# Optimization experiments

Measured on AMD Instinct MI355X. Metric: run time of the kernel, lower is better.

Reference implementation:

```python
import jax, jax.numpy as jnp
import numpy as np

B, T = 2048, 512
IN, H1, H2, D1 = 1, 128, 64, 25


def _lstm_layer(x, w_ih, w_hh, b_ih, b_hh):
    """PyTorch-style LSTM layer. x: [B,T,in], returns hidden seq [B,T,H].
    Gate order (PyTorch): i, f, g, o."""
    Bb = x.shape[0]
    H = w_hh.shape[1]
    # Precompute input projections for all timesteps: [B,T,4H]
    x_proj = jnp.einsum('bti,gi->btg', x, w_ih) + b_ih + b_hh

    def step(carry, xt):
        h, c = carry  # [B,H] each
        gates = xt + h @ w_hh.T  # [B,4H]
        i, f, g, o = jnp.split(gates, 4, axis=-1)
        i = jax.nn.sigmoid(i)
        f = jax.nn.sigmoid(f)
        g = jnp.tanh(g)
        o = jax.nn.sigmoid(o)
        c = f * c + i * g
        h = o * jnp.tanh(c)
        return (h, c), h

    h0 = jnp.zeros((Bb, H), x.dtype)
    c0 = jnp.zeros((Bb, H), x.dtype)
    (_, _), hs = jax.lax.scan(step, (h0, c0), jnp.swapaxes(x_proj, 0, 1))
    return jnp.swapaxes(hs, 0, 1)  # [B,T,H]


def setup_inputs() -> dict:
    key = jax.random.key(0)
    ks = jax.random.split(key, 13)
    s1 = 1.0 / np.sqrt(H1)
    s2 = 1.0 / np.sqrt(H2)
    sd1 = 1.0 / np.sqrt(H2)
    sd2 = 1.0 / np.sqrt(D1)
    u = lambda k, shape, s: jax.random.uniform(k, shape, jnp.float32, -s, s)
    return {
        'x': jax.random.normal(ks[0], (B, T, IN), jnp.float32),
        'w_ih1': u(ks[1], (4 * H1, IN), s1),
        'w_hh1': u(ks[2], (4 * H1, H1), s1),
        'b_ih1': u(ks[3], (4 * H1,), s1),
        'b_hh1': u(ks[4], (4 * H1,), s1),
        'w_ih2': u(ks[5], (4 * H2, H1), s2),
        'w_hh2': u(ks[6], (4 * H2, H2), s2),
        'b_ih2': u(ks[7], (4 * H2,), s2),
        'b_hh2': u(ks[8], (4 * H2,), s2),
        'w_d1': u(ks[9], (D1, H2), sd1),
        'b_d1': u(ks[10], (D1,), sd1),
        'w_d2': u(ks[11], (1, D1), sd2),
        'b_d2': u(ks[12], (1,), sd2),
    }


def reference(x, w_ih1, w_hh1, b_ih1, b_hh1, w_ih2, w_hh2, b_ih2, b_hh2,
              w_d1, b_d1, w_d2, b_d2):
    out = _lstm_layer(x, w_ih1, w_hh1, b_ih1, b_hh1)   # [B,T,128]
    out = _lstm_layer(out, w_ih2, w_hh2, b_ih2, b_hh2)  # [B,T,64]
    last = out[:, -1, :]                                 # [B,64]
    h = last @ w_d1.T + b_d1                             # [B,25]
    y = h @ w_d2.T + b_d2                                # [B,1]
    return y
```

## Files before the change

### kernel.cpp

```cpp
#include <hip/hip_runtime.h>

#define TS 512
#define LOG2E 1.4426950408889634f

typedef _Float16 f16x8 __attribute__((ext_vector_type(8)));
typedef float f32x4 __attribute__((ext_vector_type(4)));

#define MFMA16(a, b, c) __builtin_amdgcn_mfma_f32_16x16x32_f16((a), (b), (c), 0, 0, 0)

__global__ __launch_bounds__(512) void prep(
    const float* __restrict__ w_hh1, const float* __restrict__ w_ih2,
    const float* __restrict__ w_hh2, _Float16* __restrict__ wsh)
{
  int idx = blockIdx.x * 512 + threadIdx.x;
  if (idx >= 114688) return;
  int slot = idx >> 3, j = idx & 7;
  float v;
  if (slot < 8192) {
    int l = slot & 63, fi = slot >> 6;
    int w = fi >> 5, f = fi & 31, tau = f >> 2, kt = f & 3;
    int n = (tau >> 1) * 128 + w * 32 + (tau & 1) * 16 + (l & 15);
    int k = kt * 32 + (l >> 4) * 8 + j;
    v = w_hh1[n * 128 + k];
  } else {
    int s2 = slot - 8192;
    int l = s2 & 63, fi = s2 >> 6;
    int w2 = fi / 24, f = fi % 24, g = f / 6, kt = f % 6;
    int n = g * 64 + w2 * 16 + (l & 15);
    int k = kt * 32 + (l >> 4) * 8 + j;
    v = (k < 128) ? w_ih2[n * 128 + k] : w_hh2[n * 64 + (k - 128)];
  }
  wsh[idx] = (_Float16)(v * LOG2E);
}

__device__ __forceinline__ float rcpf_(float x) { return __builtin_amdgcn_rcpf(x); }
__device__ __forceinline__ float sig_s(float s)  { return rcpf_(1.0f + exp2f(-s)); }
__device__ __forceinline__ float tanh_s(float s) { return 1.0f - 2.0f * rcpf_(exp2f(s + s) + 1.0f); }
__device__ __forceinline__ float tanh_c(float c) { return 1.0f - 2.0f * rcpf_(exp2f(c * (2.0f * LOG2E)) + 1.0f); }


#define L1_BODY(I, PI, PIM)                                                    \
  {                                                                            \
    f16x8 a0 = *(const f16x8*)((PIM) + lofs);                                  \
    f16x8 a1 = *(const f16x8*)((PIM) + lofs + 1024);                           \
    f16x8 a2 = *(const f16x8*)((PIM) + lofs + 2048);                           \
    f16x8 a3 = *(const f16x8*)((PIM) + lofs + 3072);                           \
    f32x4 acc[8];                                                              \
    _Pragma("unroll") for (int tau = 0; tau < 8; ++tau) {                      \
      acc[tau] = (f32x4){biv[tau], biv[tau], biv[tau], biv[tau]};              \
      acc[tau] = MFMA16(a0, BF[tau * 4 + 0], acc[tau]);                        \
      acc[tau] = MFMA16(a1, BF[tau * 4 + 1], acc[tau]);                        \
      acc[tau] = MFMA16(a2, BF[tau * 4 + 2], acc[tau]);                        \
      acc[tau] = MFMA16(a3, BF[tau * 4 + 3], acc[tau]);                        \
    }                                                                          \
    const float xv0 = x_lds[(rb + 0) * 516 + (I)];                             \
    const float xv1 = x_lds[(rb + 1) * 516 + (I)];                             \
    _Pragma("unroll") for (int c = 0; c < 2; ++c) {                            \
      _Pragma("unroll") for (int rr = 0; rr < 2; ++rr) {                       \
        const float xv = rr ? xv1 : xv0;                                       \
        float sv[4];                                                           \
        _Pragma("unroll") for (int g = 0; g < 4; ++g) {                        \
          const int tau = g * 2 + c;                                           \
          const float oth = __shfl_xor(acc[tau][2 + rr], 32, 64);              \
          const float mine = acc[tau][rr];                                     \
          sv[g] = fmaf(xv, wxv[tau], up ? oth : mine);                         \
        }                                                                      \
        const float ii = sig_s(sv[0]), ff = sig_s(sv[1]);                      \
        const float gv = tanh_s(sv[2]), oo = sig_s(sv[3]);                     \
        const int ci = c * 2 + rr;                                             \
        cst[ci] = fmaf(ff, cst[ci], ii * gv);                                  \
        const float hv = oo * tanh_c(cst[ci]);                                 \
        *(_Float16*)((PI) + ha[ci]) = (_Float16)hv;                            \
      }                                                                        \
    }                                                                          \
  }

#define L2_BODY(PI, PIM, WRLDS, WRF)                                           \
  {                                                                            \
    f16x8 e0 = *(const f16x8*)((PIM) + lofs);                                  \
    f16x8 e1 = *(const f16x8*)((PIM) + lofs + 1024);                           \
    f16x8 e2 = *(const f16x8*)((PIM) + lofs + 2048);                           \
    f16x8 e3 = *(const f16x8*)((PIM) + lofs + 3072);                           \
    f16x8 e4 = *(const f16x8*)((PI) + lofs + 4096);                            \
    f16x8 e5 = *(const f16x8*)((PI) + lofs + 5120);                            \
    f32x4 acc[4];                                                              \
    _Pragma("unroll") for (int g = 0; g < 4; ++g) {                            \
      acc[g] = (f32x4){biv[g], biv[g], biv[g], biv[g]};                        \
      acc[g] = MFMA16(e0, BF[g * 6 + 0], acc[g]);                              \
      acc[g] = MFMA16(e1, BF[g * 6 + 1], acc[g]);                              \
      acc[g] = MFMA16(e2, BF[g * 6 + 2], acc[g]);                              \
      acc[g] = MFMA16(e3, BF[g * 6 + 3], acc[g]);                              \
      acc[g] = MFMA16(e4, BF[g * 6 + 4], acc[g]);                              \
      acc[g] = MFMA16(e5, BF[g * 6 + 5], acc[g]);                              \
    }                                                                          \
    _Pragma("unroll") for (int rr = 0; rr < 2; ++rr) {                         \
      float sv[4];                                                             \
      _Pragma("unroll") for (int g = 0; g < 4; ++g) {                          \
        const float oth = __shfl_xor(acc[g][2 + rr], 32, 64);                  \
        const float mine = acc[g][rr];                                         \
        sv[g] = up ? oth : mine;                                               \
      }                                                                        \
      const float ii = sig_s(sv[0]), ff = sig_s(sv[1]);                        \
      const float gv = tanh_s(sv[2]), oo = sig_s(sv[3]);                       \
      cst[rr] = fmaf(ff, cst[rr], ii * gv);                                    \
      const float hv = oo * tanh_c(cst[rr]);                                   \
      if (WRLDS) *(_Float16*)((PIM) + ha[rr]) = (_Float16)hv;                  \
      if (WRF) h2f[rb + rr][w2 * 16 + col] = hv;                               \
    }                                                                          \
  }

__global__ __launch_bounds__(512, 2) void lstm_mfma(
    const float* __restrict__ x,
    const float* __restrict__ w_ih1,
    const float* __restrict__ b_ih1, const float* __restrict__ b_hh1,
    const float* __restrict__ b_ih2, const float* __restrict__ b_hh2,
    const float* __restrict__ w_d1, const float* __restrict__ b_d1,
    const float* __restrict__ w_d2, const float* __restrict__ b_d2,
    const _Float16* __restrict__ wsh,
    float* __restrict__ out)
{
  __shared__ __align__(16) _Float16 HC[2 * 3072];
  __shared__ __align__(16) float x_lds[8 * 516];
  __shared__ float h2f[8][65];
  __shared__ float dh[200];

  const int tid = threadIdx.x;
  const int w   = tid >> 6;
  const int l   = tid & 63;
  const int col = l & 15;
  const int qh  = (l >> 4) & 1;
  const int up  = l >> 5;
  const int rb  = 4 * qh + 2 * up;
  const int wg  = w >> 2;
  const int w2  = w & 3;
  const int r0  = blockIdx.x * 8;
  const int lofs = l * 16;

  f16x8 BF[32];
  float biv[8], wxv[8];
  int ha[4];

  if (wg == 0) {
    #pragma unroll
    for (int f = 0; f < 32; ++f)
      BF[f] = *(const f16x8*)(wsh + ((w * 32 + f) * 64 + l) * 8);
    #pragma unroll
    for (int tau = 0; tau < 8; ++tau) {
      int u = (tau >> 1) * 128 + w * 32 + (tau & 1) * 16 + col;
      biv[tau] = (b_ih1[u] + b_hh1[u]) * LOG2E;
      wxv[tau] = w_ih1[u] * LOG2E;
    }
    #pragma unroll
    for (int c = 0; c < 2; ++c)
      #pragma unroll
      for (int rr = 0; rr < 2; ++rr) {
        int u = w * 32 + c * 16 + col;
        int r = rb + rr;
        ha[c * 2 + rr] = (u >> 5) * 1024 + (r + ((u >> 3) & 3) * 16) * 16 + (u & 7) * 2;
      }
  } else {
    #pragma unroll
    for (int f = 0; f < 24; ++f)
      BF[f] = *(const f16x8*)(wsh + 65536 + ((w2 * 24 + f) * 64 + l) * 8);
    #pragma unroll
    for (int g = 0; g < 4; ++g) {
      int u = g * 64 + w2 * 16 + col;
      biv[g] = (b_ih2[u] + b_hh2[u]) * LOG2E;
    }
    #pragma unroll
    for (int rr = 0; rr < 2; ++rr) {
      int u2 = w2 * 16 + col;
      int r = rb + rr;
      ha[rr] = (4 + (u2 >> 5)) * 1024 + (r + ((u2 >> 3) & 3) * 16) * 16 + (u2 & 7) * 2;
    }
  }

  {
    int r = tid >> 6, cc = (tid & 63) * 8;
    const float4* src = (const float4*)(x + (r0 + r) * 512 + cc);
    float4 v0 = src[0], v1 = src[1];
    *(float4*)(x_lds + r * 516 + cc)     = v0;
    *(float4*)(x_lds + r * 516 + cc + 4) = v1;
  }
  for (int i2 = tid; i2 < 3072; i2 += 512) ((unsigned*)HC)[i2] = 0u;

  float cst[4] = {0.f, 0.f, 0.f, 0.f};
  char* const hcb = (char*)HC;
  __syncthreads();

  #pragma unroll 1
  for (int i = 0; i < TS; i += 2) {
    if (wg == 0)      { L1_BODY(i, hcb, hcb + 6144) }
    else if (i > 0)   { L2_BODY(hcb, hcb + 6144, 1, 0) }
    __syncthreads();
    if (wg == 0)      { L1_BODY(i + 1, hcb + 6144, hcb) }
    else              { L2_BODY(hcb + 6144, hcb, 1, 0) }
    __syncthreads();
  }
  if (wg == 1)        { L2_BODY(hcb, hcb + 6144, 0, 1) }
  __syncthreads();

  if (tid < 200) {
    int r = tid / 25, d = tid - r * 25;
    float acc = b_d1[d];
    #pragma unroll
    for (int uu = 0; uu < 64; ++uu) acc = fmaf(h2f[r][uu], w_d1[d * 64 + uu], acc);
    dh[tid] = acc;
  }
  __syncthreads();
  if (tid < 8) {
    float y = b_d2[0];
    #pragma unroll
    for (int d = 0; d < 25; ++d) y = fmaf(dh[tid * 25 + d], w_d2[d], y);
    out[r0 + tid] = y;
  }
}

extern "C" void kernel_launch(void* const* d_in, const int* in_sizes, int n_in,
                              void* d_out, int out_size, void* d_ws, size_t ws_size,
                              hipStream_t stream) {
  (void)in_sizes; (void)n_in; (void)out_size; (void)ws_size;
  const float* x     = (const float*)d_in[0];
  const float* w_ih1 = (const float*)d_in[1];
  const float* w_hh1 = (const float*)d_in[2];
  const float* b_ih1 = (const float*)d_in[3];
  const float* b_hh1 = (const float*)d_in[4];
  const float* w_ih2 = (const float*)d_in[5];
  const float* w_hh2 = (const float*)d_in[6];
  const float* b_ih2 = (const float*)d_in[7];
  const float* b_hh2 = (const float*)d_in[8];
  const float* w_d1  = (const float*)d_in[9];
  const float* b_d1  = (const float*)d_in[10];
  const float* w_d2  = (const float*)d_in[11];
  const float* b_d2  = (const float*)d_in[12];
  _Float16* wsh = (_Float16*)d_ws;
  float* outp = (float*)d_out;

  prep<<<224, 512, 0, stream>>>(w_hh1, w_ih2, w_hh2, wsh);
  lstm_mfma<<<256, 512, 0, stream>>>(x, w_ih1, b_ih1, b_hh1, b_ih2, b_hh2,
                                     w_d1, b_d1, w_d2, b_d2, wsh, outp);
}
```

Before: 564.4 us.

## Split layer-1 across 8 waves and fold input projection and bias into MFMA

Layer 1 now runs on 8 waves instead of 4, each owning 16 hidden units, so blocks grow to 768 threads with 3 blocks per CU targeted. The scalar x*w_ih + bias term is folded into one extra MFMA by packing (1, x) as fp16 in LDS, with a prepped weight fragment holding bias and w_ih. This halves per-wave register and serial work on the layer-1 critical path and removes per-step FMA work. The cost is bias and x now rounded to fp16, more waves contending per barrier, and higher register pressure limits at 768 threads.

```diff
diff --git a/kernel.cpp b/kernel.cpp
--- a/kernel.cpp
+++ b/kernel.cpp
@@ -5,27 +5,34 @@
 
 typedef _Float16 f16x8 __attribute__((ext_vector_type(8)));
 typedef float f32x4 __attribute__((ext_vector_type(4)));
+typedef unsigned int u32;
 
 #define MFMA16(a, b, c) __builtin_amdgcn_mfma_f32_16x16x32_f16((a), (b), (c), 0, 0, 0)
 
 __global__ __launch_bounds__(512) void prep(
-    const float* __restrict__ w_hh1, const float* __restrict__ w_ih2,
-    const float* __restrict__ w_hh2, _Float16* __restrict__ wsh)
+    const float* __restrict__ w_hh1, const float* __restrict__ w_ih1,
+    const float* __restrict__ b_ih1, const float* __restrict__ b_hh1,
+    const float* __restrict__ w_ih2, const float* __restrict__ w_hh2,
+    _Float16* __restrict__ wsh)
 {
   int idx = blockIdx.x * 512 + threadIdx.x;
-  if (idx >= 114688) return;
-  int slot = idx >> 3, j = idx & 7;
+  int l = (idx >> 3) & 63, j = idx & 7;
   float v;
-  if (slot < 8192) {
-    int l = slot & 63, fi = slot >> 6;
-    int w = fi >> 5, f = fi & 31, tau = f >> 2, kt = f & 3;
-    int n = (tau >> 1) * 128 + w * 32 + (tau & 1) * 16 + (l & 15);
+  if (idx < 65536) {
+    int f = idx >> 9;
+    int wi = f >> 4, g = (f >> 2) & 3, kt = f & 3;
+    int n = g * 128 + wi * 16 + (l & 15);
     int k = kt * 32 + (l >> 4) * 8 + j;
     v = w_hh1[n * 128 + k];
+  } else if (idx < 81920) {
+    int f = (idx - 65536) >> 9;
+    int wi = f >> 2, g = f & 3;
+    int n = g * 128 + wi * 16 + (l & 15);
+    int s = (l >> 4) * 8 + j;
+    v = (s == 0) ? (b_ih1[n] + b_hh1[n]) : ((s == 1) ? w_ih1[n] : 0.0f);
   } else {
-    int s2 = slot - 8192;
-    int l = s2 & 63, fi = s2 >> 6;
-    int w2 = fi / 24, f = fi % 24, g = f / 6, kt = f % 6;
+    int f = (idx - 81920) >> 9;
+    int w2 = f / 24, rem = f % 24, g = rem / 6, kt = rem % 6;
     int n = g * 64 + w2 * 16 + (l & 15);
     int k = kt * 32 + (l >> 4) * 8 + j;
     v = (k < 128) ? w_ih2[n * 128 + k] : w_hh2[n * 64 + (k - 128)];
@@ -41,78 +48,66 @@
 
 #define L1_BODY(I, PI, PIM)                                                    \
   {                                                                            \
-    f16x8 a0 = *(const f16x8*)((PIM) + lofs);                                  \
-    f16x8 a1 = *(const f16x8*)((PIM) + lofs + 1024);                           \
-    f16x8 a2 = *(const f16x8*)((PIM) + lofs + 2048);                           \
-    f16x8 a3 = *(const f16x8*)((PIM) + lofs + 3072);                           \
-    f32x4 acc[8];                                                              \
-    _Pragma("unroll") for (int tau = 0; tau < 8; ++tau) {                      \
-      acc[tau] = (f32x4){biv[tau], biv[tau], biv[tau], biv[tau]};              \
-      acc[tau] = MFMA16(a0, BF[tau * 4 + 0], acc[tau]);                        \
-      acc[tau] = MFMA16(a1, BF[tau * 4 + 1], acc[tau]);                        \
-      acc[tau] = MFMA16(a2, BF[tau * 4 + 2], acc[tau]);                        \
-      acc[tau] = MFMA16(a3, BF[tau * 4 + 3], acc[tau]);                        \
-    }                                                                          \
-    const float xv0 = x_lds[(rb + 0) * 516 + (I)];                             \
-    const float xv1 = x_lds[(rb + 1) * 516 + (I)];                             \
-    _Pragma("unroll") for (int c = 0; c < 2; ++c) {                            \
-      _Pragma("unroll") for (int rr = 0; rr < 2; ++rr) {                       \
-        const float xv = rr ? xv1 : xv0;                                       \
-        float sv[4];                                                           \
-        _Pragma("unroll") for (int g = 0; g < 4; ++g) {                        \
-          const int tau = g * 2 + c;                                           \
-          const float oth = __shfl_xor(acc[tau][2 + rr], 32, 64);              \
-          const float mine = acc[tau][rr];                                     \
-          sv[g] = fmaf(xv, wxv[tau], up ? oth : mine);                         \
-        }                                                                      \
-        const float ii = sig_s(sv[0]), ff = sig_s(sv[1]);                      \
-        const float gv = tanh_s(sv[2]), oo = sig_s(sv[3]);                     \
-        const int ci = c * 2 + rr;                                             \
-        cst[ci] = fmaf(ff, cst[ci], ii * gv);                                  \
-        const float hv = oo * tanh_c(cst[ci]);                                 \
-        *(_Float16*)((PI) + ha[ci]) = (_Float16)hv;                            \
-      }                                                                        \
-    }                                                                          \
-  }
-
-#define L2_BODY(PI, PIM, WRLDS, WRF)                                           \
-  {                                                                            \
-    f16x8 e0 = *(const f16x8*)((PIM) + lofs);                                  \
-    f16x8 e1 = *(const f16x8*)((PIM) + lofs + 1024);                           \
-    f16x8 e2 = *(const f16x8*)((PIM) + lofs + 2048);                           \
-    f16x8 e3 = *(const f16x8*)((PIM) + lofs + 3072);                           \
-    f16x8 e4 = *(const f16x8*)((PI) + lofs + 4096);                            \
-    f16x8 e5 = *(const f16x8*)((PI) + lofs + 5120);                            \
+    union { u32 uu[4]; f16x8 vv; } a6u;                                        \
+    a6u.uu[0] = xpk[xrow + (I)];                                               \
+    a6u.uu[1] = 0u; a6u.uu[2] = 0u; a6u.uu[3] = 0u;                            \
     f32x4 acc[4];                                                              \
-    _Pragma("unroll") for (int g = 0; g < 4; ++g) {                            \
-      acc[g] = (f32x4){biv[g], biv[g], biv[g], biv[g]};                        \
-      acc[g] = MFMA16(e0, BF[g * 6 + 0], acc[g]);                              \
-      acc[g] = MFMA16(e1, BF[g * 6 + 1], acc[g]);                              \
-      acc[g] = MFMA16(e2, BF[g * 6 + 2], acc[g]);                              \
-      acc[g] = MFMA16(e3, BF[g * 6 + 3], acc[g]);                              \
-      acc[g] = MFMA16(e4, BF[g * 6 + 4], acc[g]);                              \
-      acc[g] = MFMA16(e5, BF[g * 6 + 5], acc[g]);                              \
+    _Pragma("unroll") for (int g = 0; g < 4; ++g)                              \
+      acc[g] = MFMA16(a6u.vv, BF[16 + g], zq);                                 \
+    _Pragma("unroll") for (int kt = 0; kt < 4; ++kt) {                         \
+      f16x8 av = *(const f16x8*)((PIM) + lofs + kt * 1024);                    \
+      _Pragma("unroll") for (int g = 0; g < 4; ++g)                            \
+        acc[g] = MFMA16(av, BF[g * 4 + kt], acc[g]);                           \
     }                                                                          \
     _Pragma("unroll") for (int rr = 0; rr < 2; ++rr) {                         \
       float sv[4];                                                             \
       _Pragma("unroll") for (int g = 0; g < 4; ++g) {                          \
         const float oth = __shfl_xor(acc[g][2 + rr], 32, 64);                  \
-        const float mine = acc[g][rr];                                         \
-        sv[g] = up ? oth : mine;                                               \
+        sv[g] = up ? oth : acc[g][rr];                                         \
+      }                                                                        \
+      const float ii = sig_s(sv[0]), ff = sig_s(sv[1]);                        \
+      const float gv = tanh_s(sv[2]), oo = sig_s(sv[3]);                       \
+      cst[rr] = fmaf(ff, cst[rr], ii * gv);                                    \
+      const float hv = oo * tanh_c(cst[rr]);                                   \
+      *(_Float16*)((PI) + ha[rr]) = (_Float16)hv;                              \
+    }                                                                          \
+  }
+
+#define L2_BODY(PI, PIM, WRLDS, WRF)                                           \
+  {                                                                            \
+    f32x4 acc[4];                                                              \
+    {                                                                          \
+      f16x8 ev = *(const f16x8*)((PIM) + lofs);                                \
+      _Pragma("unroll") for (int g = 0; g < 4; ++g)                            \
+        acc[g] = MFMA16(ev, BF[g * 6], zq);                                    \
+    }                                                                          \
+    _Pragma("unroll") for (int kt = 1; kt < 4; ++kt) {                         \
+      f16x8 ev = *(const f16x8*)((PIM) + lofs + kt * 1024);                    \
+      _Pragma("unroll") for (int g = 0; g < 4; ++g)                            \
+        acc[g] = MFMA16(ev, BF[g * 6 + kt], acc[g]);                           \
+    }                                                                          \
+    _Pragma("unroll") for (int kt = 4; kt < 6; ++kt) {                         \
+      f16x8 ev = *(const f16x8*)((PI) + lofs + kt * 1024);                     \
+      _Pragma("unroll") for (int g = 0; g < 4; ++g)                            \
+        acc[g] = MFMA16(ev, BF[g * 6 + kt], acc[g]);                           \
+    }                                                                          \
+    _Pragma("unroll") for (int rr = 0; rr < 2; ++rr) {                         \
+      float sv[4];                                                             \
+      _Pragma("unroll") for (int g = 0; g < 4; ++g) {                          \
+        const float oth = __shfl_xor(acc[g][2 + rr], 32, 64);                  \
+        sv[g] = (up ? oth : acc[g][rr]) + biv[g];                              \
       }                                                                        \
       const float ii = sig_s(sv[0]), ff = sig_s(sv[1]);                        \
       const float gv = tanh_s(sv[2]), oo = sig_s(sv[3]);                       \
       cst[rr] = fmaf(ff, cst[rr], ii * gv);                                    \
       const float hv = oo * tanh_c(cst[rr]);                                   \
       if (WRLDS) *(_Float16*)((PIM) + ha[rr]) = (_Float16)hv;                  \
-      if (WRF) h2f[rb + rr][w2 * 16 + col] = hv;                               \
-    }                                                                          \
-  }
-
-__global__ __launch_bounds__(512, 2) void lstm_mfma(
+      if (WRF) h2f[rb + rr][u2] = hv;                                          \
+    }                                                                          \
+  }
+
+__global__ __launch_bounds__(768, 3) void lstm_mfma(
     const float* __restrict__ x,
-    const float* __restrict__ w_ih1,
-    const float* __restrict__ b_ih1, const float* __restrict__ b_hh1,
     const float* __restrict__ b_ih2, const float* __restrict__ b_hh2,
     const float* __restrict__ w_d1, const float* __restrict__ b_d1,
     const float* __restrict__ w_d2, const float* __restrict__ b_d2,
@@ -120,7 +115,7 @@
     float* __restrict__ out)
 {
   __shared__ __align__(16) _Float16 HC[2 * 3072];
-  __shared__ __align__(16) float x_lds[8 * 516];
+  __shared__ __align__(16) u32 xpk[8 * 516];
   __shared__ float h2f[8][65];
   __shared__ float dh[200];
 
@@ -128,63 +123,53 @@
   const int w   = tid >> 6;
   const int l   = tid & 63;
   const int col = l & 15;
-  const int qh  = (l >> 4) & 1;
-  const int up  = l >> 5;
-  const int rb  = 4 * qh + 2 * up;
-  const int wg  = w >> 2;
-  const int w2  = w & 3;
+  const int q   = l >> 4;
+  const int up  = q >> 1;
+  const int rb  = 4 * (q & 1) + 2 * up;
+  const int wg  = (w < 8) ? 0 : 1;
+  const int w2  = w - 8;
   const int r0  = blockIdx.x * 8;
   const int lofs = l * 16;
-
-  f16x8 BF[32];
-  float biv[8], wxv[8];
-  int ha[4];
+  const int xrow = (l & 7) * 516;
+  const int u2  = (wg == 1) ? (w2 * 16 + col) : 0;
+
+  f16x8 BF[24];
+  float biv[4] = {0.f, 0.f, 0.f, 0.f};
+  int ha[2];
 
   if (wg == 0) {
     #pragma unroll
-    for (int f = 0; f < 32; ++f)
-      BF[f] = *(const f16x8*)(wsh + ((w * 32 + f) * 64 + l) * 8);
-    #pragma unroll
-    for (int tau = 0; tau < 8; ++tau) {
-      int u = (tau >> 1) * 128 + w * 32 + (tau & 1) * 16 + col;
-      biv[tau] = (b_ih1[u] + b_hh1[u]) * LOG2E;
-      wxv[tau] = w_ih1[u] * LOG2E;
-    }
-    #pragma unroll
-    for (int c = 0; c < 2; ++c)
-      #pragma unroll
-      for (int rr = 0; rr < 2; ++rr) {
-        int u = w * 32 + c * 16 + col;
-        int r = rb + rr;
-        ha[c * 2 + rr] = (u >> 5) * 1024 + (r + ((u >> 3) & 3) * 16) * 16 + (u & 7) * 2;
-      }
+    for (int f = 0; f < 16; ++f)
+      BF[f] = *(const f16x8*)(wsh + (w * 16 + f) * 512 + l * 8);
+    #pragma unroll
+    for (int g = 0; g < 4; ++g)
+      BF[16 + g] = *(const f16x8*)(wsh + 65536 + (w * 4 + g) * 512 + l * 8);
+    const int u = w * 16 + col;
+    #pragma unroll
+    for (int rr = 0; rr < 2; ++rr)
+      ha[rr] = (u >> 5) * 1024 + ((rb + rr) + ((u >> 3) & 3) * 16) * 16 + (u & 7) * 2;
   } else {
     #pragma unroll
     for (int f = 0; f < 24; ++f)
-      BF[f] = *(const f16x8*)(wsh + 65536 + ((w2 * 24 + f) * 64 + l) * 8);
-    #pragma unroll
-    for (int g = 0; g < 4; ++g) {
-      int u = g * 64 + w2 * 16 + col;
-      biv[g] = (b_ih2[u] + b_hh2[u]) * LOG2E;
-    }
-    #pragma unroll
-    for (int rr = 0; rr < 2; ++rr) {
-      int u2 = w2 * 16 + col;
-      int r = rb + rr;
-      ha[rr] = (4 + (u2 >> 5)) * 1024 + (r + ((u2 >> 3) & 3) * 16) * 16 + (u2 & 7) * 2;
-    }
-  }
-
-  {
-    int r = tid >> 6, cc = (tid & 63) * 8;
-    const float4* src = (const float4*)(x + (r0 + r) * 512 + cc);
-    float4 v0 = src[0], v1 = src[1];
-    *(float4*)(x_lds + r * 516 + cc)     = v0;
-    *(float4*)(x_lds + r * 516 + cc + 4) = v1;
-  }
-  for (int i2 = tid; i2 < 3072; i2 += 512) ((unsigned*)HC)[i2] = 0u;
-
-  float cst[4] = {0.f, 0.f, 0.f, 0.f};
+      BF[f] = *(const f16x8*)(wsh + 81920 + (w2 * 24 + f) * 512 + l * 8);
+    #pragma unroll
+    for (int g = 0; g < 4; ++g)
+      biv[g] = (b_ih2[g * 64 + u2] + b_hh2[g * 64 + u2]) * LOG2E;
+    #pragma unroll
+    for (int rr = 0; rr < 2; ++rr)
+      ha[rr] = (4 + (u2 >> 5)) * 1024 + ((rb + rr) + ((u2 >> 3) & 3) * 16) * 16 + (u2 & 7) * 2;
+  }
+
+  for (int i = tid; i < 4096; i += 768) {
+    int r = i >> 9, t = i & 511;
+    union { _Float16 h; unsigned short s; } cv;
+    cv.h = (_Float16)x[(r0 + r) * 512 + t];
+    xpk[r * 516 + t] = 0x3C00u | ((u32)cv.s << 16);
+  }
+  for (int i = tid; i < 3072; i += 768) ((u32*)HC)[i] = 0u;
+
+  float cst[2] = {0.f, 0.f};
+  const f32x4 zq = {0.f, 0.f, 0.f, 0.f};
   char* const hcb = (char*)HC;
   __syncthreads();
 
@@ -236,7 +221,6 @@
   _Float16* wsh = (_Float16*)d_ws;
   float* outp = (float*)d_out;
 
-  prep<<<224, 512, 0, stream>>>(w_hh1, w_ih2, w_hh2, wsh);
-  lstm_mfma<<<256, 512, 0, stream>>>(x, w_ih1, b_ih1, b_hh1, b_ih2, b_hh2,
-                                     w_d1, b_d1, w_d2, b_d2, wsh, outp);
+  prep<<<256, 512, 0, stream>>>(w_hh1, w_ih1, b_ih1, b_hh1, w_ih2, w_hh2, wsh);
+  lstm_mfma<<<256, 768, 0, stream>>>(x, b_ih2, b_hh2, w_d1, b_d1, w_d2, b_d2, wsh, outp);
 }
```

Measured after the change: 573.8 us. No clear change (+1.7%).
